# Performance work log

Measured on AMD Instinct MI355X. Metric: run time of the kernel, lower is better.

Reference implementation:

```python
import jax, jax.numpy as jnp
import numpy as np

H = 128          # hidden_channels == num_features for both node types
L = 3            # num_layers
E_TYPES = 3      # (a->a), (a->b), (b->a)
N = 200000       # nodes per type
E = 600000       # edges per edge type
G = 64           # graphs in batch
C = 10           # num_classes
BN_EPS = 1e-5


def setup_inputs() -> dict:
    key = jax.random.key(0)
    ks = jax.random.split(key, 16)
    x_a = jax.random.normal(ks[0], (N, H), dtype=jnp.float32)
    x_b = jax.random.normal(ks[1], (N, H), dtype=jnp.float32)
    ei_aa = jax.random.randint(ks[2], (2, E), 0, N, dtype=jnp.int32)
    ei_ab = jax.random.randint(ks[3], (2, E), 0, N, dtype=jnp.int32)
    ei_ba = jax.random.randint(ks[4], (2, E), 0, N, dtype=jnp.int32)
    batch_a = jnp.sort(jax.random.randint(ks[5], (N,), 0, G, dtype=jnp.int32))
    batch_b = jnp.sort(jax.random.randint(ks[6], (N,), 0, G, dtype=jnp.int32))
    s = 1.0 / np.sqrt(H)
    # GraphConv params per (layer, edge_type): lin_rel (weight+bias), lin_root (no bias)
    Wrel = jax.random.uniform(ks[7], (L, E_TYPES, H, H), jnp.float32, -s, s)
    brel = jax.random.uniform(ks[8], (L, E_TYPES, H), jnp.float32, -s, s)
    Wroot = jax.random.uniform(ks[9], (L, E_TYPES, H, H), jnp.float32, -s, s)
    # BatchNorm affine params per node type (0='a', 1='b')
    bn_gamma = jnp.ones((2, H), jnp.float32)
    bn_beta = jnp.zeros((2, H), jnp.float32)
    lin_W = jax.random.uniform(ks[10], (C, H), jnp.float32, -s, s)
    lin_b = jax.random.uniform(ks[11], (C,), jnp.float32, -s, s)
    return {"x_a": x_a, "x_b": x_b, "Wrel": Wrel, "brel": brel, "Wroot": Wroot,
            "bn_gamma": bn_gamma, "bn_beta": bn_beta, "lin_W": lin_W, "lin_b": lin_b,
            "ei_aa": ei_aa, "ei_ab": ei_ab, "ei_ba": ei_ba,
            "batch_a": batch_a, "batch_b": batch_b}


def _graph_conv(x_src, x_dst, ei, W_rel, b_rel, W_root):
    # PyG GraphConv (aggr='add'): out = lin_rel(sum_{j in N(i)} x_j) + lin_root(x_i)
    agg = jax.ops.segment_sum(x_src[ei[0]], ei[1], num_segments=x_dst.shape[0])
    return agg @ W_rel.T + b_rel + x_dst @ W_root.T


def _bn(x, gamma, beta):
    # BatchNorm in training mode: batch statistics (biased variance)
    mu = x.mean(axis=0)
    var = x.var(axis=0)
    return gamma * (x - mu) * jax.lax.rsqrt(var + BN_EPS) + beta


def reference(x_a, x_b, Wrel, brel, Wroot, bn_gamma, bn_beta, lin_W, lin_b,
              ei_aa, ei_ab, ei_ba, batch_a, batch_b):
    for l in range(L):
        # HeteroConv sums contributions per destination node type
        out_a = (_graph_conv(x_a, x_a, ei_aa, Wrel[l, 0], brel[l, 0], Wroot[l, 0]) +
                 _graph_conv(x_b, x_a, ei_ba, Wrel[l, 2], brel[l, 2], Wroot[l, 2]))
        out_b = _graph_conv(x_a, x_b, ei_ab, Wrel[l, 1], brel[l, 1], Wroot[l, 1])
        x_a = _bn(jax.nn.relu(out_a), bn_gamma[0], bn_beta[0])
        x_b = _bn(jax.nn.relu(out_b), bn_gamma[1], bn_beta[1])
    # global mean pool over concatenated node types
    feats = jnp.concatenate([x_a, x_b], axis=0)
    batch = jnp.concatenate([batch_a, batch_b], axis=0)
    sums = jax.ops.segment_sum(feats, batch, num_segments=G)
    counts = jax.ops.segment_sum(jnp.ones((feats.shape[0],), feats.dtype), batch, num_segments=G)
    pooled = sums / jnp.maximum(counts, 1.0)[:, None]
    return pooled @ lin_W.T + lin_b
```

## Files before the change

### kernel.cpp

```cpp
#include <hip/hip_runtime.h>
#include <hip/hip_bf16.h>

#define HF 128

typedef unsigned int uint32;
typedef unsigned short ushort16;
typedef float f32x4 __attribute__((ext_vector_type(4)));
typedef __bf16 bf16x8 __attribute__((ext_vector_type(8)));

__device__ __forceinline__ float bflo(uint32 u) { return __uint_as_float(u << 16); }
__device__ __forceinline__ float bfhi(uint32 u) { return __uint_as_float(u & 0xffff0000u); }
__device__ __forceinline__ ushort16 f2bf(float f) {
  uint32 u = __float_as_uint(f);
  return (ushort16)((u + 0x7fffu + ((u >> 16) & 1u)) >> 16);
}
__device__ __forceinline__ uint32 pack2(float lo, float hi) {
  return (uint32)f2bf(lo) | ((uint32)f2bf(hi) << 16);
}

__global__ void diag_k(float* __restrict__ out, int n, float val) {
  int i = blockIdx.x * 256 + threadIdx.x;
  if (i < n) out[i] = val;
}

__global__ void init_k(float* __restrict__ ss, float* __restrict__ pool, int Gn) {
  int idx = blockIdx.x * 256 + threadIdx.x;
  if (idx < 512) ss[idx] = (idx < 128 || (idx >= 256 && idx < 384)) ? 1.f : 0.f;
  int p = idx - 512;
  if (p >= 0 && p < Gn * HF) pool[p] = 0.f;
}

__global__ void zrow_k(uint32* __restrict__ a0, uint32* __restrict__ a1,
                       uint32* __restrict__ b, size_t offA, size_t offB) {
  int t = threadIdx.x;
  if (t < 64) a0[offA + t] = 0;
  else if (t < 128) a1[offA + (t - 64)] = 0;
  else if (t < 192) b[offB + (t - 128)] = 0;
}

__global__ void conv_k(const float* __restrict__ in, uint32* __restrict__ out, int n4) {
  int i = blockIdx.x * 256 + threadIdx.x;
  if (i >= n4) return;
  float4 v = ((const float4*)in)[i];
  uint2 p;
  p.x = pack2(v.x, v.y);
  p.y = pack2(v.z, v.w);
  ((uint2*)out)[i] = p;
}

__global__ void initcs_k(int* __restrict__ cs, size_t c0, size_t c1, size_t c2,
                         int vA, int vB) {
  size_t i = ((size_t)blockIdx.x * 256 + threadIdx.x) * 4;
  size_t tot = c0 + c1 + c2;
  if (i >= tot) return;
  int v = (i < c0 + c1) ? vA : vB;
  int4 w = make_int4(v, v, v, v);
  *(int4*)&cs[i] = w;
}

__global__ void count3_k(const int* __restrict__ eA, int EA, int* __restrict__ rA,
                         const int* __restrict__ eB, int EB, int* __restrict__ rB,
                         const int* __restrict__ eC, int EC, int* __restrict__ rC,
                         int B0, int B1) {
  int b = blockIdx.x;
  const int* ei; int E; int* rp;
  if (b < B0)            { ei = eA; E = EA; rp = rA; }
  else if (b < B0 + B1)  { ei = eB; E = EB; rp = rB; b -= B0; }
  else                   { ei = eC; E = EC; rp = rC; b -= B0 + B1; }
  int e = b * 256 + threadIdx.x;
  if (e < E) atomicAdd(&rp[ei[E + e]], 1);
}

__device__ __forceinline__ int pad4(int c) { return (c + 3) & ~3; }

__device__ __forceinline__ void scan1_body(const int* __restrict__ rp, int N,
                                           int* __restrict__ bsum, int b, int t) {
  int i = b * 1024 + t * 4;
  int s = 0;
  if (i + 3 < N) {
    int4 v = *(const int4*)&rp[i];
    s = pad4(v.x) + pad4(v.y) + pad4(v.z) + pad4(v.w);
  } else {
    for (int j = 0; j < 4; ++j) if (i + j < N) s += pad4(rp[i + j]);
  }
  __shared__ int sd[256];
  sd[t] = s;
  __syncthreads();
  for (int o = 128; o > 0; o >>= 1) {
    if (t < o) sd[t] += sd[t + o];
    __syncthreads();
  }
  if (t == 0) bsum[b] = sd[0];
}

__global__ __launch_bounds__(256) void scan1x3_k(
    const int* __restrict__ rA, int NA, int* __restrict__ bA,
    const int* __restrict__ rB, int NB, int* __restrict__ bB,
    const int* __restrict__ rC, int NC, int* __restrict__ bC, int nbA, int nbB) {
  int b = blockIdx.x;
  if (b < nbA)            scan1_body(rA, NA, bA, b, threadIdx.x);
  else if (b < nbA + nbB) scan1_body(rB, NB, bB, b - nbA, threadIdx.x);
  else                    scan1_body(rC, NC, bC, b - nbA - nbB, threadIdx.x);
}

__global__ __launch_bounds__(1024) void scan2x3_k(int* __restrict__ bA, int nbA,
                                                  int* __restrict__ bB, int nbB,
                                                  int* __restrict__ bC, int nbC) {
  int* bsum = (blockIdx.x == 0) ? bA : (blockIdx.x == 1) ? bB : bC;
  int nb    = (blockIdx.x == 0) ? nbA : (blockIdx.x == 1) ? nbB : nbC;
  __shared__ int sd[1024];
  int t = threadIdx.x;
  int v = (t < nb) ? bsum[t] : 0;
  sd[t] = v;
  __syncthreads();
  for (int o = 1; o < 1024; o <<= 1) {
    int x = (t >= o) ? sd[t - o] : 0;
    __syncthreads();
    sd[t] += x;
    __syncthreads();
  }
  if (t < nb) bsum[t] = sd[t] - v;
}

__device__ __forceinline__ void scan3_body(int* __restrict__ rp, int* __restrict__ cur,
                                           int* __restrict__ deg,
                                           const int* __restrict__ bsum, int N,
                                           int b, int t) {
  int i = b * 1024 + t * 4;
  int c[4];
  #pragma unroll
  for (int j = 0; j < 4; ++j) c[j] = (i + j < N) ? rp[i + j] : 0;
  int tsum = pad4(c[0]) + pad4(c[1]) + pad4(c[2]) + pad4(c[3]);
  __shared__ int sd[256];
  sd[t] = tsum;
  __syncthreads();
  for (int o = 1; o < 256; o <<= 1) {
    int x = (t >= o) ? sd[t - o] : 0;
    __syncthreads();
    sd[t] += x;
    __syncthreads();
  }
  int off = bsum[b] + sd[t] - tsum;
  int p = off;
  #pragma unroll
  for (int j = 0; j < 4; ++j) {
    if (i + j < N) { rp[i + j] = p; cur[i + j] = p; deg[i + j] = c[j]; }
    p += pad4(c[j]);
  }
  if (i < N && N <= i + 4) rp[N] = off + tsum;
}

__global__ __launch_bounds__(256) void scan3x3_k(
    int* __restrict__ rA, int* __restrict__ cA, int* __restrict__ dA,
    const int* __restrict__ bA, int NA,
    int* __restrict__ rB, int* __restrict__ cB, int* __restrict__ dB,
    const int* __restrict__ bB, int NB,
    int* __restrict__ rC, int* __restrict__ cC, int* __restrict__ dC,
    const int* __restrict__ bC, int NC,
    int nbA, int nbB) {
  int b = blockIdx.x;
  if (b < nbA)            scan3_body(rA, cA, dA, bA, NA, b, threadIdx.x);
  else if (b < nbA + nbB) scan3_body(rB, cB, dB, bB, NB, b - nbA, threadIdx.x);
  else                    scan3_body(rC, cC, dC, bC, NC, b - nbA - nbB, threadIdx.x);
}

#define FILL_P 4
__global__ __launch_bounds__(256) void fill3p_k(
    const int* __restrict__ eA, int EA, int* __restrict__ cuA, int* __restrict__ csA,
    const int* __restrict__ eB, int EB, int* __restrict__ cuB, int* __restrict__ csB,
    const int* __restrict__ eC, int EC, int* __restrict__ cuC, int* __restrict__ csC,
    int NA, int NBn, int B0, int B1, int Btot) {
  int pass = blockIdx.x / Btot;
  int b = blockIdx.x % Btot;
  const int* ei; int E; int* cur; int* cs; int N;
  if (b < B0)           { ei = eA; E = EA; cur = cuA; cs = csA; N = NA; }
  else if (b < B0 + B1) { ei = eB; E = EB; cur = cuB; cs = csB; N = NBn; b -= B0; }
  else                  { ei = eC; E = EC; cur = cuC; cs = csC; N = NA; b -= B0 + B1; }
  int e = b * 256 + threadIdx.x;
  if (e >= E) return;
  int dst = ei[E + e];
  int lo = (int)(((long long)pass * N) / FILL_P);
  int hi = (int)(((long long)(pass + 1) * N) / FILL_P);
  if (dst < lo || dst >= hi) return;
  int pos = atomicAdd(&cur[dst], 1);
  cs[pos] = ei[e];
}

__global__ __launch_bounds__(128) void prep2_k(
    const float* __restrict__ Wrel_l, const float* __restrict__ Wroot_l,
    const float* __restrict__ brel_l, const float* __restrict__ ss,
    ushort16* __restrict__ BWa, ushort16* __restrict__ BWb,
    float* __restrict__ uvec, float* __restrict__ stats) {
  __shared__ float red[128];
  int n = blockIdx.x, k = threadIdx.x;
  if (n < 64) {
    float4 z = make_float4(0.f, 0.f, 0.f, 0.f);
    *(float4*)&stats[n * 512 + k * 4] = z;
  }
  float scA = ss[k], shA = ss[128 + k], scB = ss[256 + k], shB = ss[384 + k];
  float w0  = Wrel_l[n * HF + k];
  float w1  = Wrel_l[16384 + n * HF + k];
  float w2  = Wrel_l[32768 + n * HF + k];
  float wr1 = Wroot_l[16384 + n * HF + k];
  float wrc = Wroot_l[n * HF + k] + Wroot_l[32768 + n * HF + k];

  int ksl = k >> 5;
  int lane = (n & 15) + (((k >> 3) & 3) << 4);
  int j = k & 7;
  int nt = n >> 4;
  auto put = [&](ushort16* B, int ksb, float v) {
    B[((size_t)((ksb + ksl) * 8 + nt) * 64 + lane) * 8 + j] = f2bf(v);
  };
  put(BWa, 0, scA * w0);
  put(BWa, 4, scB * w2);
  put(BWa, 8, scA * wrc);
  put(BWb, 0, scA * w1);
  put(BWb, 4, scB * wr1);

  auto reduce = [&](float v) -> float {
    red[k] = v;
    __syncthreads();
    for (int s = 64; s > 0; s >>= 1) {
      if (k < s) red[k] += red[k + s];
      __syncthreads();
    }
    float r = red[0];
    __syncthreads();
    return r;
  };
  float r0 = reduce(shA * w0);
  float r1 = reduce(shB * w2);
  float r2 = reduce(shA * w1);
  float r3 = reduce(shA * wrc);
  float r4 = reduce(shB * wr1);
  if (k == 0) {
    uvec[n]       = r0;
    uvec[128 + n] = r1;
    uvec[256 + n] = r2;
    uvec[384 + n] = brel_l[n] + brel_l[256 + n] + r3;
    uvec[512 + n] = brel_l[128 + n] + r4;
  }
}

template <bool HAS2>
__global__ __launch_bounds__(256) void gg_k(
    const uint32* __restrict__ Xg1, const int* __restrict__ rp1, const int* __restrict__ cs1,
    const int* __restrict__ deg1,
    const uint32* __restrict__ Xg2, const int* __restrict__ rp2, const int* __restrict__ cs2,
    const int* __restrict__ deg2,
    const uint32* Xr,
    const bf16x8* __restrict__ BW,
    const float* __restrict__ u1, const float* __restrict__ u2,
    const float* __restrict__ bias,
    uint32* out,
    float* __restrict__ statS, float* __restrict__ statQ,
    int nRows) {
  constexpr int KS_G = HAS2 ? 8 : 4;
  __shared__ uint32 lds[4][1088];
  int tid = threadIdx.x, wid = tid >> 6, l = tid & 63;
  int R0 = blockIdx.x * 64 + wid * 16;
  uint32* L = &lds[wid][0];
  int row = l & 15, khi = l >> 4;
  int myRow = R0 + row;
  bool okRow = myRow < nRows;
  int rowIdx = okRow ? myRow : nRows;

  float lo[16], hi[16];
  auto addv = [&](int base, uint4 v) {
    hi[base + 0] += __uint_as_float(v.x); lo[base + 0] += __uint_as_float(v.x << 16);
    hi[base + 1] += __uint_as_float(v.y); lo[base + 1] += __uint_as_float(v.y << 16);
    hi[base + 2] += __uint_as_float(v.z); lo[base + 2] += __uint_as_float(v.z << 16);
    hi[base + 3] += __uint_as_float(v.w); lo[base + 3] += __uint_as_float(v.w << 16);
  };
  auto gather_reg = [&](const uint32* __restrict__ Xg, const int* __restrict__ rp,
                        const int* __restrict__ cs) {
    #pragma unroll
    for (int i = 0; i < 16; ++i) { lo[i] = 0.f; hi[i] = 0.f; }
    if (okRow) {
      int e0 = rp[myRow], e1 = rp[myRow + 1];
      for (int e = e0; e < e1; e += 4) {
        int i0 = cs[e], i1 = cs[e + 1], i2 = cs[e + 2], i3 = cs[e + 3];
        const uint32* p0 = &Xg[(size_t)i0 * 64 + khi * 4];
        const uint32* p1 = &Xg[(size_t)i1 * 64 + khi * 4];
        const uint32* p2 = &Xg[(size_t)i2 * 64 + khi * 4];
        const uint32* p3 = &Xg[(size_t)i3 * 64 + khi * 4];
        uint4 a0 = *(const uint4*)&p0[0];
        uint4 a1 = *(const uint4*)&p0[16];
        uint4 a2 = *(const uint4*)&p0[32];
        uint4 a3 = *(const uint4*)&p0[48];
        uint4 b0 = *(const uint4*)&p1[0];
        uint4 b1 = *(const uint4*)&p1[16];
        uint4 b2 = *(const uint4*)&p1[32];
        uint4 b3 = *(const uint4*)&p1[48];
        uint4 c0 = *(const uint4*)&p2[0];
        uint4 c1 = *(const uint4*)&p2[16];
        uint4 c2 = *(const uint4*)&p2[32];
        uint4 c3 = *(const uint4*)&p2[48];
        uint4 d0 = *(const uint4*)&p3[0];
        uint4 d1 = *(const uint4*)&p3[16];
        uint4 d2 = *(const uint4*)&p3[32];
        uint4 d3 = *(const uint4*)&p3[48];
        addv(0, a0); addv(4, a1); addv(8, a2); addv(12, a3);
        addv(0, b0); addv(4, b1); addv(8, b2); addv(12, b3);
        addv(0, c0); addv(4, c1); addv(8, c2); addv(12, c3);
        addv(0, d0); addv(4, d1); addv(8, d2); addv(12, d3);
      }
    }
  };
  auto to_frag = [&](int ks) -> bf16x8 {
    bf16x8 a;
    #pragma unroll
    for (int j = 0; j < 4; ++j) {
      a[2 * j]     = (__bf16)lo[ks * 4 + j];
      a[2 * j + 1] = (__bf16)hi[ks * 4 + j];
    }
    return a;
  };

  f32x4 acc[8] = {};
  const bf16x8* Bl = BW + l;

  gather_reg(Xg1, rp1, cs1);
  {
    bf16x8 af[4];
    #pragma unroll
    for (int ks = 0; ks < 4; ++ks) af[ks] = to_frag(ks);
    #pragma unroll
    for (int ks = 0; ks < 4; ++ks) {
      #pragma unroll
      for (int nt = 0; nt < 8; ++nt) {
        bf16x8 b = Bl[(size_t)(ks * 8 + nt) * 64];
        acc[nt] = __builtin_amdgcn_mfma_f32_16x16x32_bf16(af[ks], b, acc[nt], 0, 0, 0);
      }
    }
  }
  if constexpr (HAS2) {
    gather_reg(Xg2, rp2, cs2);
    bf16x8 af[4];
    #pragma unroll
    for (int ks = 0; ks < 4; ++ks) af[ks] = to_frag(ks);
    #pragma unroll
    for (int ks = 0; ks < 4; ++ks) {
      #pragma unroll
      for (int nt = 0; nt < 8; ++nt) {
        bf16x8 b = Bl[(size_t)((4 + ks) * 8 + nt) * 64];
        acc[nt] = __builtin_amdgcn_mfma_f32_16x16x32_bf16(af[ks], b, acc[nt], 0, 0, 0);
      }
    }
  }
  #pragma unroll
  for (int ks = 0; ks < 4; ++ks) {
    bf16x8 a = *(const bf16x8*)&Xr[(size_t)rowIdx * 64 + (ks * 4 + khi) * 4];
    #pragma unroll
    for (int nt = 0; nt < 8; ++nt) {
      bf16x8 b = Bl[(size_t)((KS_G + ks) * 8 + nt) * 64];
      acc[nt] = __builtin_amdgcn_mfma_f32_16x16x32_bf16(a, b, acc[nt], 0, 0, 0);
    }
  }

  int rl0 = khi * 4;
  float deg1v[4], deg2v[4];
  #pragma unroll
  for (int j = 0; j < 4; ++j) {
    int r = R0 + rl0 + j;
    deg1v[j] = (r < nRows) ? (float)deg1[r] : 0.f;
    if constexpr (HAS2) deg2v[j] = (r < nRows) ? (float)deg2[r] : 0.f;
    else deg2v[j] = 0.f;
  }
  ushort16* P = (ushort16*)L;
  int c0 = l & 15;
  float ps[8], pq[8];
  #pragma unroll
  for (int nt = 0; nt < 8; ++nt) {
    int col = nt * 16 + c0;
    float bc = bias[col];
    float u1c = u1[col];
    float u2c = HAS2 ? u2[col] : 0.f;
    float s = 0.f, q = 0.f;
    #pragma unroll
    for (int j = 0; j < 4; ++j) {
      float v = acc[nt][j] + bc + deg1v[j] * u1c;
      if constexpr (HAS2) v += deg2v[j] * u2c;
      v = fmaxf(v, 0.f);
      if (R0 + rl0 + j < nRows) { s += v; q += v * v; }
      P[(rl0 + j) * 136 + col] = f2bf(v);
    }
    ps[nt] = s; pq[nt] = q;
  }

  #pragma unroll
  for (int rr = 0; rr < 4; ++rr) {
    int rloc = rr * 4 + khi;
    int grow = R0 + rloc;
    if (grow < nRows) {
      uint4 v = *(const uint4*)&P[rloc * 136 + c0 * 8];
      *(uint4*)&out[(size_t)grow * 64 + c0 * 4] = v;
    }
  }

  #pragma unroll
  for (int nt = 0; nt < 8; ++nt) {
    ps[nt] += __shfl_xor(ps[nt], 16); ps[nt] += __shfl_xor(ps[nt], 32);
    pq[nt] += __shfl_xor(pq[nt], 16); pq[nt] += __shfl_xor(pq[nt], 32);
  }
  if (l < 16) {
    float* S = statS + (size_t)(blockIdx.x & 63) * 128;
    float* Q = statQ + (size_t)(blockIdx.x & 63) * 128;
    #pragma unroll
    for (int nt = 0; nt < 8; ++nt) {
      unsafeAtomicAdd(&S[nt * 16 + l], ps[nt]);
      unsafeAtomicAdd(&Q[nt * 16 + l], pq[nt]);
    }
  }
}

__global__ void bn_fin_k(const float* __restrict__ stats, const float* __restrict__ gamma,
                         const float* __restrict__ beta, float* __restrict__ ss,
                         float nA, float nB) {
  int t = threadIdx.x;
  if (t >= 256) return;
  int type = t >> 7, f = t & 127;
  const float* S = stats + (size_t)type * 16384;
  const float* Q = S + 8192;
  float s = 0.f, q = 0.f;
  for (int st = 0; st < 64; ++st) { s += S[st * 128 + f]; q += Q[st * 128 + f]; }
  float nN = type ? nB : nA;
  float mean = s / nN;
  float var = q / nN - mean * mean;
  float rstd = rsqrtf(var + 1e-5f);
  float sc = gamma[type * HF + f] * rstd;
  float sh = beta[type * HF + f] - mean * sc;
  ss[type * 256 + f] = sc;
  ss[type * 256 + 128 + f] = sh;
}

__global__ __launch_bounds__(256) void pool_k(const uint32* __restrict__ x,
                                              const int* __restrict__ batch,
                                              const float* __restrict__ scale,
                                              const float* __restrict__ shift,
                                              float* __restrict__ pool, int nN) {
  int f2 = threadIdx.x & 31;
  int sub = threadIdx.x >> 5;
  int start = blockIdx.x * 1024;
  int end = min(start + 1024, nN);
  float4 sc = *(const float4*)&scale[f2 * 4];
  float4 sh = *(const float4*)&shift[f2 * 4];
  float a0 = 0.f, a1 = 0.f, a2 = 0.f, a3 = 0.f, cnt = 0.f;
  int cur = -1;
  for (int n = start + sub; n < end; n += 8) {
    int g = batch[n];
    if (g != cur) {
      if (cur >= 0) {
        float* bp = &pool[(size_t)cur * HF + f2 * 4];
        unsafeAtomicAdd(bp + 0, sc.x * a0 + cnt * sh.x);
        unsafeAtomicAdd(bp + 1, sc.y * a1 + cnt * sh.y);
        unsafeAtomicAdd(bp + 2, sc.z * a2 + cnt * sh.z);
        unsafeAtomicAdd(bp + 3, sc.w * a3 + cnt * sh.w);
      }
      a0 = a1 = a2 = a3 = 0.f; cnt = 0.f; cur = g;
    }
    uint2 v = *(const uint2*)&x[(size_t)n * 64 + f2 * 2];
    a0 += bflo(v.x); a1 += bfhi(v.x); a2 += bflo(v.y); a3 += bfhi(v.y);
    cnt += 1.f;
  }
  if (cur >= 0) {
    float* bp = &pool[(size_t)cur * HF + f2 * 4];
    unsafeAtomicAdd(bp + 0, sc.x * a0 + cnt * sh.x);
    unsafeAtomicAdd(bp + 1, sc.y * a1 + cnt * sh.y);
    unsafeAtomicAdd(bp + 2, sc.z * a2 + cnt * sh.z);
    unsafeAtomicAdd(bp + 3, sc.w * a3 + cnt * sh.w);
  }
}

__device__ inline int lowerb(const int* a, int n, int v) {
  int lo = 0, hi = n;
  while (lo < hi) { int m = (lo + hi) >> 1; if (a[m] < v) lo = m + 1; else hi = m; }
  return lo;
}

__global__ void counts_k(const int* __restrict__ ba, int nA, const int* __restrict__ bb, int nB,
                         float* __restrict__ counts, int Gn) {
  for (int g = threadIdx.x; g < Gn; g += blockDim.x) {
    int c = (lowerb(ba, nA, g + 1) - lowerb(ba, nA, g)) +
            (lowerb(bb, nB, g + 1) - lowerb(bb, nB, g));
    counts[g] = fmaxf((float)c, 1.f);
  }
}

__global__ void final_k(const float* __restrict__ pool, const float* __restrict__ counts,
                        const float* __restrict__ linW, const float* __restrict__ linb,
                        float* __restrict__ out, int Cn) {
  int g = blockIdx.x;
  int lane = threadIdx.x;
  float inv = 1.f / counts[g];
  float p0 = pool[(size_t)g * HF + lane] * inv;
  float p1 = pool[(size_t)g * HF + 64 + lane] * inv;
  for (int c = 0; c < Cn; ++c) {
    float t = p0 * linW[c * HF + lane] + p1 * linW[c * HF + 64 + lane];
    for (int off = 32; off > 0; off >>= 1) t += __shfl_down(t, off);
    if (lane == 0) out[g * Cn + c] = t + linb[c];
  }
}

extern "C" void kernel_launch(void* const* d_in, const int* in_sizes, int n_in,
                              void* d_out, int out_size, void* d_ws, size_t ws_size,
                              hipStream_t stream) {
  const float* x_a   = (const float*)d_in[0];
  const float* x_b   = (const float*)d_in[1];
  const float* Wrel  = (const float*)d_in[2];
  const float* brel  = (const float*)d_in[3];
  const float* Wroot = (const float*)d_in[4];
  const float* bn_g  = (const float*)d_in[5];
  const float* bn_b  = (const float*)d_in[6];
  const float* lin_W = (const float*)d_in[7];
  const float* lin_b = (const float*)d_in[8];
  const int* ei_aa   = (const int*)d_in[9];
  const int* ei_ab   = (const int*)d_in[10];
  const int* ei_ba   = (const int*)d_in[11];
  const int* batch_a = (const int*)d_in[12];
  const int* batch_b = (const int*)d_in[13];

  int Na  = in_sizes[0] / HF;
  int Nb  = in_sizes[1] / HF;
  int Eaa = in_sizes[9] / 2;
  int Eab = in_sizes[10] / 2;
  int Eba = in_sizes[11] / 2;
  int Cn  = in_sizes[7] / HF;
  int Gn  = out_size / Cn;

  size_t NHa = (size_t)Na * HF, NHb = (size_t)Nb * HF;
  size_t capA = ((size_t)Eaa + 3 * (size_t)Na + 15) & ~(size_t)15;
  size_t capB = ((size_t)Eab + 3 * (size_t)Nb + 15) & ~(size_t)15;
  size_t capC = ((size_t)Eba + 3 * (size_t)Na + 15) & ~(size_t)15;

  char* base = (char*)d_ws;
  auto alignup = [](size_t x) { return (x + 255) & ~(size_t)255; };
  size_t off = 0;
  size_t oXA0 = off; off = alignup(off + (NHa + HF) * 2);
  size_t oXA1 = off; off = alignup(off + (NHa + HF) * 2);
  size_t oXB  = off; off = alignup(off + (NHb + HF) * 2);
  size_t oRP  = off; off = alignup(off + ((size_t)(Na + 1) + (Nb + 1) + (Na + 1)) * 4);
  size_t oCUR = off; off = alignup(off + ((size_t)Na + Nb + Na) * 4);
  size_t oDEG = off; off = alignup(off + ((size_t)Na + Nb + Na) * 4);
  size_t oCS  = off; off = alignup(off + (capA + capB + capC) * 4);
  size_t oBWA = off; off = alignup(off + (size_t)12 * 8 * 64 * 16);
  size_t oBWB = off; off = alignup(off + (size_t)8 * 8 * 64 * 16);
  size_t oUV  = off; off = alignup(off + 5 * 128 * 4);
  size_t oSS  = off; off = alignup(off + 512 * 4);
  size_t oST  = off; off = alignup(off + 32768 * 4);
  size_t oBS  = off; off = alignup(off + 3072 * 4);
  size_t oPOOL= off; off = alignup(off + (size_t)Gn * HF * 4);
  size_t oCNT = off; off = alignup(off + (size_t)Gn * 4);
  size_t need = off;

  if (ws_size < need) {
    diag_k<<<(out_size + 255) / 256, 256, 0, stream>>>(
        (float*)d_out, out_size, (float)((double)ws_size / 1048576.0));
    return;
  }

  uint32* XA0 = (uint32*)(base + oXA0);
  uint32* XA1 = (uint32*)(base + oXA1);
  uint32* XB  = (uint32*)(base + oXB);
  int* rp_aa = (int*)(base + oRP);
  int* rp_ab = rp_aa + (Na + 1);
  int* rp_ba = rp_ab + (Nb + 1);
  int* cur_aa = (int*)(base + oCUR);
  int* cur_ab = cur_aa + Na;
  int* cur_ba = cur_ab + Nb;
  int* deg_aa = (int*)(base + oDEG);
  int* deg_ab = deg_aa + Na;
  int* deg_ba = deg_ab + Nb;
  int* cs_aa = (int*)(base + oCS);
  int* cs_ab = cs_aa + capA;
  int* cs_ba = cs_ab + capB;
  ushort16* BWa = (ushort16*)(base + oBWA);
  ushort16* BWb = (ushort16*)(base + oBWB);
  float* uvec  = (float*)(base + oUV);
  float* ss    = (float*)(base + oSS);
  float* stats = (float*)(base + oST);
  int* bsum    = (int*)(base + oBS);
  float* pool  = (float*)(base + oPOOL);
  float* counts= (float*)(base + oCNT);

  float* ss_a = ss;
  float* ss_b = ss + 256;
  float* uaa = uvec, *uba = uvec + 128, *uab = uvec + 256;
  float* bias_a = uvec + 384, *bias_b = uvec + 512;
  float* SA = stats, *QA = stats + 8192, *SB = stats + 16384, *QB = stats + 24576;

  init_k<<<(512 + Gn * HF + 255) / 256, 256, 0, stream>>>(ss, pool, Gn);
  conv_k<<<((int)(NHa / 4) + 255) / 256, 256, 0, stream>>>(x_a, XA0, (int)(NHa / 4));
  conv_k<<<((int)(NHb / 4) + 255) / 256, 256, 0, stream>>>(x_b, XB, (int)(NHb / 4));
  zrow_k<<<1, 256, 0, stream>>>(XA0, XA1, XB, NHa / 2, NHb / 2);

  hipMemsetAsync(rp_aa, 0, ((size_t)(Na + 1) + (Nb + 1) + (Na + 1)) * 4, stream);
  int B0 = (Eaa + 255) / 256, B1 = (Eab + 255) / 256, B2 = (Eba + 255) / 256;
  count3_k<<<B0 + B1 + B2, 256, 0, stream>>>(ei_aa, Eaa, rp_aa, ei_ab, Eab, rp_ab,
                                             ei_ba, Eba, rp_ba, B0, B1);

  int nb_a = (Na + 1023) / 1024;
  int nb_b = (Nb + 1023) / 1024;
  scan1x3_k<<<nb_a + nb_b + nb_a, 256, 0, stream>>>(
      rp_aa, Na, bsum, rp_ab, Nb, bsum + 1024, rp_ba, Na, bsum + 2048, nb_a, nb_b);
  scan2x3_k<<<3, 1024, 0, stream>>>(bsum, nb_a, bsum + 1024, nb_b, bsum + 2048, nb_a);
  scan3x3_k<<<nb_a + nb_b + nb_a, 256, 0, stream>>>(
      rp_aa, cur_aa, deg_aa, bsum, Na,
      rp_ab, cur_ab, deg_ab, bsum + 1024, Nb,
      rp_ba, cur_ba, deg_ba, bsum + 2048, Na, nb_a, nb_b);

  size_t capTot = capA + capB + capC;
  initcs_k<<<(int)((capTot / 4 + 255) / 256), 256, 0, stream>>>(
      cs_aa, capA, capB, capC, Na, Nb);

  int Btot = B0 + B1 + B2;
  fill3p_k<<<FILL_P * Btot, 256, 0, stream>>>(ei_aa, Eaa, cur_aa, cs_aa,
                                              ei_ab, Eab, cur_ab, cs_ab,
                                              ei_ba, Eba, cur_ba, cs_ba,
                                              Na, Nb, B0, B1, Btot);

  uint32* xa_cur = XA0;
  uint32* xa_nxt = XA1;
  for (int l = 0; l < 3; ++l) {
    const float* Wrel_l  = Wrel  + (size_t)l * 3 * 16384;
    const float* Wroot_l = Wroot + (size_t)l * 3 * 16384;
    const float* brel_l  = brel  + (size_t)l * 3 * HF;

    prep2_k<<<128, 128, 0, stream>>>(Wrel_l, Wroot_l, brel_l, ss, BWa, BWb, uvec, stats);

    gg_k<true><<<(Na + 63) / 64, 256, 0, stream>>>(
        xa_cur, rp_aa, cs_aa, deg_aa, XB, rp_ba, cs_ba, deg_ba, xa_cur,
        (const bf16x8*)BWa, uaa, uba, bias_a, xa_nxt, SA, QA, Na);
    gg_k<false><<<(Nb + 63) / 64, 256, 0, stream>>>(
        xa_cur, rp_ab, cs_ab, deg_ab, nullptr, nullptr, nullptr, nullptr, XB,
        (const bf16x8*)BWb, uab, nullptr, bias_b, XB, SB, QB, Nb);

    bn_fin_k<<<1, 256, 0, stream>>>(stats, bn_g, bn_b, ss, (float)Na, (float)Nb);

    uint32* t = xa_cur; xa_cur = xa_nxt; xa_nxt = t;
  }

  pool_k<<<(Na + 1023) / 1024, 256, 0, stream>>>(xa_cur, batch_a, ss_a, ss_a + 128, pool, Na);
  pool_k<<<(Nb + 1023) / 1024, 256, 0, stream>>>(XB, batch_b, ss_b, ss_b + 128, pool, Nb);
  counts_k<<<1, 256, 0, stream>>>(batch_a, Na, batch_b, Nb, counts, Gn);
  final_k<<<Gn, 64, 0, stream>>>(pool, counts, lin_W, lin_b, (float*)d_out, Cn);
}
```

Before: 1.088 ms.

## Fuse setup and BN-finalize kernels, prefetch edge indices in gather

Merges the input-conversion, dummy-row zeroing, CSR index init and pool zeroing kernels into one setup launch. BatchNorm finalization moves into the weight-prep kernel by double-buffering the stats, and graph counts fold into the final linear kernel, cutting per-layer and tail launches. The gather-GEMM kernel now loads CSR neighbour indices as int4 with one-step-ahead prefetch and hoists root-row and degree loads ahead of the gathers to overlap latency. In exchange, prep2 redundantly reduces stats in every block, and register pressure rises from holding both A fragments at once.

```diff
diff --git a/kernel.cpp b/kernel.cpp
--- a/kernel.cpp
+++ b/kernel.cpp
@@ -23,39 +23,54 @@
   if (i < n) out[i] = val;
 }
 
-__global__ void init_k(float* __restrict__ ss, float* __restrict__ pool, int Gn) {
-  int idx = blockIdx.x * 256 + threadIdx.x;
-  if (idx < 512) ss[idx] = (idx < 128 || (idx >= 256 && idx < 384)) ? 1.f : 0.f;
-  int p = idx - 512;
-  if (p >= 0 && p < Gn * HF) pool[p] = 0.f;
-}
-
-__global__ void zrow_k(uint32* __restrict__ a0, uint32* __restrict__ a1,
-                       uint32* __restrict__ b, size_t offA, size_t offB) {
-  int t = threadIdx.x;
-  if (t < 64) a0[offA + t] = 0;
-  else if (t < 128) a1[offA + (t - 64)] = 0;
-  else if (t < 192) b[offB + (t - 128)] = 0;
-}
-
-__global__ void conv_k(const float* __restrict__ in, uint32* __restrict__ out, int n4) {
-  int i = blockIdx.x * 256 + threadIdx.x;
-  if (i >= n4) return;
-  float4 v = ((const float4*)in)[i];
-  uint2 p;
-  p.x = pack2(v.x, v.y);
-  p.y = pack2(v.z, v.w);
-  ((uint2*)out)[i] = p;
-}
-
-__global__ void initcs_k(int* __restrict__ cs, size_t c0, size_t c1, size_t c2,
-                         int vA, int vB) {
-  size_t i = ((size_t)blockIdx.x * 256 + threadIdx.x) * 4;
-  size_t tot = c0 + c1 + c2;
-  if (i >= tot) return;
-  int v = (i < c0 + c1) ? vA : vB;
-  int4 w = make_int4(v, v, v, v);
-  *(int4*)&cs[i] = w;
+__global__ __launch_bounds__(256) void setup_k(
+    const float* __restrict__ xa, const float* __restrict__ xb,
+    uint32* __restrict__ XA0, uint32* __restrict__ XA1, uint32* __restrict__ XB,
+    int n4a, int n4b,
+    int* __restrict__ cs, size_t capA, size_t capB, size_t capC, int vA, int vB,
+    float* __restrict__ pool, int poolN4,
+    size_t dummyA, size_t dummyB,
+    int CA, int CB, int CI, int PZ) {
+  int b = blockIdx.x, t = threadIdx.x;
+  if (b < CA) {
+    int i = b * 256 + t;
+    if (i < n4a) {
+      float4 v = ((const float4*)xa)[i];
+      uint2 p; p.x = pack2(v.x, v.y); p.y = pack2(v.z, v.w);
+      ((uint2*)XA0)[i] = p;
+    }
+    return;
+  }
+  b -= CA;
+  if (b < CB) {
+    int i = b * 256 + t;
+    if (i < n4b) {
+      float4 v = ((const float4*)xb)[i];
+      uint2 p; p.x = pack2(v.x, v.y); p.y = pack2(v.z, v.w);
+      ((uint2*)XB)[i] = p;
+    }
+    return;
+  }
+  b -= CB;
+  if (b < CI) {
+    size_t i = ((size_t)b * 256 + t) * 4;
+    size_t tot = capA + capB + capC;
+    if (i < tot) {
+      int v = (i < capA + capB) ? vA : vB;
+      int4 w = make_int4(v, v, v, v);
+      *(int4*)&cs[i] = w;
+    }
+    return;
+  }
+  b -= CI;
+  if (b < PZ) {
+    int i = b * 256 + t;
+    if (i < poolN4) ((float4*)pool)[i] = make_float4(0.f, 0.f, 0.f, 0.f);
+    return;
+  }
+  if (t < 64) XA0[dummyA + t] = 0;
+  else if (t < 128) XA1[dummyA + (t - 64)] = 0;
+  else if (t < 192) XB[dummyB + (t - 128)] = 0;
 }
 
 __global__ void count3_k(const int* __restrict__ eA, int EA, int* __restrict__ rA,
@@ -188,16 +203,36 @@
 
 __global__ __launch_bounds__(128) void prep2_k(
     const float* __restrict__ Wrel_l, const float* __restrict__ Wroot_l,
-    const float* __restrict__ brel_l, const float* __restrict__ ss,
+    const float* __restrict__ brel_l,
+    const float* __restrict__ gamma, const float* __restrict__ beta,
+    const float* __restrict__ statsPrev, float* __restrict__ statsNext,
+    float nA, float nB, int first,
     ushort16* __restrict__ BWa, ushort16* __restrict__ BWb,
-    float* __restrict__ uvec, float* __restrict__ stats) {
+    float* __restrict__ uvec) {
   __shared__ float red[128];
   int n = blockIdx.x, k = threadIdx.x;
+  float scA, shA, scB, shB;
+  if (first) {
+    scA = 1.f; shA = 0.f; scB = 1.f; shB = 0.f;
+  } else {
+    float sA = 0.f, qA = 0.f, sB = 0.f, qB = 0.f;
+    for (int st = 0; st < 64; ++st) {
+      sA += statsPrev[st * 128 + k];
+      qA += statsPrev[8192 + st * 128 + k];
+      sB += statsPrev[16384 + st * 128 + k];
+      qB += statsPrev[24576 + st * 128 + k];
+    }
+    float mA = sA / nA, vA = qA / nA - mA * mA;
+    float rA = rsqrtf(vA + 1e-5f);
+    scA = gamma[k] * rA; shA = beta[k] - mA * scA;
+    float mB = sB / nB, vB = qB / nB - mB * mB;
+    float rB = rsqrtf(vB + 1e-5f);
+    scB = gamma[128 + k] * rB; shB = beta[128 + k] - mB * scB;
+  }
   if (n < 64) {
     float4 z = make_float4(0.f, 0.f, 0.f, 0.f);
-    *(float4*)&stats[n * 512 + k * 4] = z;
-  }
-  float scA = ss[k], shA = ss[128 + k], scB = ss[256 + k], shB = ss[384 + k];
+    *(float4*)&statsNext[n * 512 + k * 4] = z;
+  }
   float w0  = Wrel_l[n * HF + k];
   float w1  = Wrel_l[16384 + n * HF + k];
   float w2  = Wrel_l[32768 + n * HF + k];
@@ -265,6 +300,28 @@
   bool okRow = myRow < nRows;
   int rowIdx = okRow ? myRow : nRows;
 
+  int e0a = 0, e1a = 0;
+  if (okRow) { e0a = rp1[myRow]; e1a = rp1[myRow + 1]; }
+  int e0b = 0, e1b = 0;
+  if constexpr (HAS2) { if (okRow) { e0b = rp2[myRow]; e1b = rp2[myRow + 1]; } }
+  bf16x8 rt[4];
+  #pragma unroll
+  for (int ks = 0; ks < 4; ++ks)
+    rt[ks] = *(const bf16x8*)&Xr[(size_t)rowIdx * 64 + (ks * 4 + khi) * 4];
+  int4 q1 = make_int4(0, 0, 0, 0), q2 = make_int4(0, 0, 0, 0);
+  if (e0a < e1a) q1 = *(const int4*)&cs1[e0a];
+  if constexpr (HAS2) { if (e0b < e1b) q2 = *(const int4*)&cs2[e0b]; }
+  int rl0 = khi * 4;
+  float dg1[4] = {0.f, 0.f, 0.f, 0.f}, dg2[4] = {0.f, 0.f, 0.f, 0.f};
+  #pragma unroll
+  for (int j = 0; j < 4; ++j) {
+    int r = R0 + rl0 + j;
+    if (r < nRows) {
+      dg1[j] = (float)deg1[r];
+      if constexpr (HAS2) dg2[j] = (float)deg2[r];
+    }
+  }
+
   float lo[16], hi[16];
   auto addv = [&](int base, uint4 v) {
     hi[base + 0] += __uint_as_float(v.x); lo[base + 0] += __uint_as_float(v.x << 16);
@@ -272,39 +329,44 @@
     hi[base + 2] += __uint_as_float(v.z); lo[base + 2] += __uint_as_float(v.z << 16);
     hi[base + 3] += __uint_as_float(v.w); lo[base + 3] += __uint_as_float(v.w << 16);
   };
-  auto gather_reg = [&](const uint32* __restrict__ Xg, const int* __restrict__ rp,
-                        const int* __restrict__ cs) {
+  auto run_tile = [&](const uint32* __restrict__ Xg, const int* __restrict__ cs,
+                      int e0, int e1, int4 qinit) {
     #pragma unroll
     for (int i = 0; i < 16; ++i) { lo[i] = 0.f; hi[i] = 0.f; }
-    if (okRow) {
-      int e0 = rp[myRow], e1 = rp[myRow + 1];
-      for (int e = e0; e < e1; e += 4) {
-        int i0 = cs[e], i1 = cs[e + 1], i2 = cs[e + 2], i3 = cs[e + 3];
-        const uint32* p0 = &Xg[(size_t)i0 * 64 + khi * 4];
-        const uint32* p1 = &Xg[(size_t)i1 * 64 + khi * 4];
-        const uint32* p2 = &Xg[(size_t)i2 * 64 + khi * 4];
-        const uint32* p3 = &Xg[(size_t)i3 * 64 + khi * 4];
-        uint4 a0 = *(const uint4*)&p0[0];
-        uint4 a1 = *(const uint4*)&p0[16];
-        uint4 a2 = *(const uint4*)&p0[32];
-        uint4 a3 = *(const uint4*)&p0[48];
-        uint4 b0 = *(const uint4*)&p1[0];
-        uint4 b1 = *(const uint4*)&p1[16];
-        uint4 b2 = *(const uint4*)&p1[32];
-        uint4 b3 = *(const uint4*)&p1[48];
-        uint4 c0 = *(const uint4*)&p2[0];
-        uint4 c1 = *(const uint4*)&p2[16];
-        uint4 c2 = *(const uint4*)&p2[32];
-        uint4 c3 = *(const uint4*)&p2[48];
-        uint4 d0 = *(const uint4*)&p3[0];
-        uint4 d1 = *(const uint4*)&p3[16];
-        uint4 d2 = *(const uint4*)&p3[32];
-        uint4 d3 = *(const uint4*)&p3[48];
-        addv(0, a0); addv(4, a1); addv(8, a2); addv(12, a3);
-        addv(0, b0); addv(4, b1); addv(8, b2); addv(12, b3);
-        addv(0, c0); addv(4, c1); addv(8, c2); addv(12, c3);
-        addv(0, d0); addv(4, d1); addv(8, d2); addv(12, d3);
-      }
+    if (e0 >= e1) return;
+    int e = e0;
+    int4 q = qinit;
+    for (;;) {
+      const uint32* p0 = &Xg[(size_t)q.x * 64 + khi * 4];
+      const uint32* p1 = &Xg[(size_t)q.y * 64 + khi * 4];
+      const uint32* p2 = &Xg[(size_t)q.z * 64 + khi * 4];
+      const uint32* p3 = &Xg[(size_t)q.w * 64 + khi * 4];
+      uint4 a0 = *(const uint4*)&p0[0];
+      uint4 a1 = *(const uint4*)&p0[16];
+      uint4 a2 = *(const uint4*)&p0[32];
+      uint4 a3 = *(const uint4*)&p0[48];
+      uint4 b0 = *(const uint4*)&p1[0];
+      uint4 b1 = *(const uint4*)&p1[16];
+      uint4 b2 = *(const uint4*)&p1[32];
+      uint4 b3 = *(const uint4*)&p1[48];
+      uint4 c0 = *(const uint4*)&p2[0];
+      uint4 c1 = *(const uint4*)&p2[16];
+      uint4 c2 = *(const uint4*)&p2[32];
+      uint4 c3 = *(const uint4*)&p2[48];
+      uint4 d0 = *(const uint4*)&p3[0];
+      uint4 d1 = *(const uint4*)&p3[16];
+      uint4 d2 = *(const uint4*)&p3[32];
+      uint4 d3 = *(const uint4*)&p3[48];
+      int en = e + 4;
+      bool more = en < e1;
+      int4 qn = q;
+      if (more) qn = *(const int4*)&cs[en];
+      addv(0, a0); addv(4, a1); addv(8, a2); addv(12, a3);
+      addv(0, b0); addv(4, b1); addv(8, b2); addv(12, b3);
+      addv(0, c0); addv(4, c1); addv(8, c2); addv(12, c3);
+      addv(0, d0); addv(4, d1); addv(8, d2); addv(12, d3);
+      if (!more) break;
+      e = en; q = qn;
     }
   };
   auto to_frag = [&](int ks) -> bf16x8 {
@@ -317,56 +379,47 @@
     return a;
   };
 
+  run_tile(Xg1, cs1, e0a, e1a, q1);
+  bf16x8 af1[4];
+  #pragma unroll
+  for (int ks = 0; ks < 4; ++ks) af1[ks] = to_frag(ks);
+
+  bf16x8 af2[4];
+  if constexpr (HAS2) {
+    run_tile(Xg2, cs2, e0b, e1b, q2);
+    #pragma unroll
+    for (int ks = 0; ks < 4; ++ks) af2[ks] = to_frag(ks);
+  }
+
   f32x4 acc[8] = {};
   const bf16x8* Bl = BW + l;
-
-  gather_reg(Xg1, rp1, cs1);
-  {
-    bf16x8 af[4];
+  #pragma unroll
+  for (int ks = 0; ks < 4; ++ks) {
     #pragma unroll
-    for (int ks = 0; ks < 4; ++ks) af[ks] = to_frag(ks);
-    #pragma unroll
-    for (int ks = 0; ks < 4; ++ks) {
-      #pragma unroll
-      for (int nt = 0; nt < 8; ++nt) {
-        bf16x8 b = Bl[(size_t)(ks * 8 + nt) * 64];
-        acc[nt] = __builtin_amdgcn_mfma_f32_16x16x32_bf16(af[ks], b, acc[nt], 0, 0, 0);
-      }
+    for (int nt = 0; nt < 8; ++nt) {
+      bf16x8 b = Bl[(size_t)(ks * 8 + nt) * 64];
+      acc[nt] = __builtin_amdgcn_mfma_f32_16x16x32_bf16(af1[ks], b, acc[nt], 0, 0, 0);
     }
   }
   if constexpr (HAS2) {
-    gather_reg(Xg2, rp2, cs2);
-    bf16x8 af[4];
-    #pragma unroll
-    for (int ks = 0; ks < 4; ++ks) af[ks] = to_frag(ks);
     #pragma unroll
     for (int ks = 0; ks < 4; ++ks) {
       #pragma unroll
       for (int nt = 0; nt < 8; ++nt) {
         bf16x8 b = Bl[(size_t)((4 + ks) * 8 + nt) * 64];
-        acc[nt] = __builtin_amdgcn_mfma_f32_16x16x32_bf16(af[ks], b, acc[nt], 0, 0, 0);
+        acc[nt] = __builtin_amdgcn_mfma_f32_16x16x32_bf16(af2[ks], b, acc[nt], 0, 0, 0);
       }
     }
   }
   #pragma unroll
   for (int ks = 0; ks < 4; ++ks) {
-    bf16x8 a = *(const bf16x8*)&Xr[(size_t)rowIdx * 64 + (ks * 4 + khi) * 4];
     #pragma unroll
     for (int nt = 0; nt < 8; ++nt) {
       bf16x8 b = Bl[(size_t)((KS_G + ks) * 8 + nt) * 64];
-      acc[nt] = __builtin_amdgcn_mfma_f32_16x16x32_bf16(a, b, acc[nt], 0, 0, 0);
-    }
-  }
-
-  int rl0 = khi * 4;
-  float deg1v[4], deg2v[4];
-  #pragma unroll
-  for (int j = 0; j < 4; ++j) {
-    int r = R0 + rl0 + j;
-    deg1v[j] = (r < nRows) ? (float)deg1[r] : 0.f;
-    if constexpr (HAS2) deg2v[j] = (r < nRows) ? (float)deg2[r] : 0.f;
-    else deg2v[j] = 0.f;
-  }
+      acc[nt] = __builtin_amdgcn_mfma_f32_16x16x32_bf16(rt[ks], b, acc[nt], 0, 0, 0);
+    }
+  }
+
   ushort16* P = (ushort16*)L;
   int c0 = l & 15;
   float ps[8], pq[8];
@@ -379,8 +432,8 @@
     float s = 0.f, q = 0.f;
     #pragma unroll
     for (int j = 0; j < 4; ++j) {
-      float v = acc[nt][j] + bc + deg1v[j] * u1c;
-      if constexpr (HAS2) v += deg2v[j] * u2c;
+      float v = acc[nt][j] + bc + dg1[j] * u1c;
+      if constexpr (HAS2) v += dg2[j] * u2c;
       v = fmaxf(v, 0.f);
       if (R0 + rl0 + j < nRows) { s += v; q += v * v; }
       P[(rl0 + j) * 136 + col] = f2bf(v);
@@ -478,27 +531,22 @@
   return lo;
 }
 
-__global__ void counts_k(const int* __restrict__ ba, int nA, const int* __restrict__ bb, int nB,
-                         float* __restrict__ counts, int Gn) {
-  for (int g = threadIdx.x; g < Gn; g += blockDim.x) {
-    int c = (lowerb(ba, nA, g + 1) - lowerb(ba, nA, g)) +
-            (lowerb(bb, nB, g + 1) - lowerb(bb, nB, g));
-    counts[g] = fmaxf((float)c, 1.f);
-  }
-}
-
-__global__ void final_k(const float* __restrict__ pool, const float* __restrict__ counts,
+__global__ void final_k(const float* __restrict__ pool,
+                        const int* __restrict__ ba, int nA,
+                        const int* __restrict__ bb, int nB,
                         const float* __restrict__ linW, const float* __restrict__ linb,
                         float* __restrict__ out, int Cn) {
   int g = blockIdx.x;
   int lane = threadIdx.x;
-  float inv = 1.f / counts[g];
+  int c = (lowerb(ba, nA, g + 1) - lowerb(ba, nA, g)) +
+          (lowerb(bb, nB, g + 1) - lowerb(bb, nB, g));
+  float inv = 1.f / fmaxf((float)c, 1.f);
   float p0 = pool[(size_t)g * HF + lane] * inv;
   float p1 = pool[(size_t)g * HF + 64 + lane] * inv;
-  for (int c = 0; c < Cn; ++c) {
-    float t = p0 * linW[c * HF + lane] + p1 * linW[c * HF + 64 + lane];
+  for (int cc = 0; cc < Cn; ++cc) {
+    float t = p0 * linW[cc * HF + lane] + p1 * linW[cc * HF + 64 + lane];
     for (int off = 32; off > 0; off >>= 1) t += __shfl_down(t, off);
-    if (lane == 0) out[g * Cn + c] = t + linb[c];
+    if (lane == 0) out[g * Cn + cc] = t + linb[cc];
   }
 }
 
@@ -547,10 +595,9 @@
   size_t oBWB = off; off = alignup(off + (size_t)8 * 8 * 64 * 16);
   size_t oUV  = off; off = alignup(off + 5 * 128 * 4);
   size_t oSS  = off; off = alignup(off + 512 * 4);
-  size_t oST  = off; off = alignup(off + 32768 * 4);
+  size_t oST  = off; off = alignup(off + 65536 * 4);
   size_t oBS  = off; off = alignup(off + 3072 * 4);
   size_t oPOOL= off; off = alignup(off + (size_t)Gn * HF * 4);
-  size_t oCNT = off; off = alignup(off + (size_t)Gn * 4);
   size_t need = off;
 
   if (ws_size < need) {
@@ -581,18 +628,22 @@
   float* stats = (float*)(base + oST);
   int* bsum    = (int*)(base + oBS);
   float* pool  = (float*)(base + oPOOL);
-  float* counts= (float*)(base + oCNT);
 
   float* ss_a = ss;
   float* ss_b = ss + 256;
   float* uaa = uvec, *uba = uvec + 128, *uab = uvec + 256;
   float* bias_a = uvec + 384, *bias_b = uvec + 512;
-  float* SA = stats, *QA = stats + 8192, *SB = stats + 16384, *QB = stats + 24576;
-
-  init_k<<<(512 + Gn * HF + 255) / 256, 256, 0, stream>>>(ss, pool, Gn);
-  conv_k<<<((int)(NHa / 4) + 255) / 256, 256, 0, stream>>>(x_a, XA0, (int)(NHa / 4));
-  conv_k<<<((int)(NHb / 4) + 255) / 256, 256, 0, stream>>>(x_b, XB, (int)(NHb / 4));
-  zrow_k<<<1, 256, 0, stream>>>(XA0, XA1, XB, NHa / 2, NHb / 2);
+
+  int n4a = (int)(NHa / 4), n4b = (int)(NHb / 4);
+  int CA = (n4a + 255) / 256, CB = (n4b + 255) / 256;
+  size_t capTot = capA + capB + capC;
+  int CI = (int)((capTot / 4 + 255) / 256);
+  int poolN4 = Gn * HF / 4;
+  int PZ = (poolN4 + 255) / 256;
+  setup_k<<<CA + CB + CI + PZ + 1, 256, 0, stream>>>(
+      x_a, x_b, XA0, XA1, XB, n4a, n4b,
+      cs_aa, capA, capB, capC, Na, Nb,
+      pool, poolN4, NHa / 2, NHb / 2, CA, CB, CI, PZ);
 
   hipMemsetAsync(rp_aa, 0, ((size_t)(Na + 1) + (Nb + 1) + (Na + 1)) * 4, stream);
   int B0 = (Eaa + 255) / 256, B1 = (Eab + 255) / 256, B2 = (Eba + 255) / 256;
@@ -609,10 +660,6 @@
       rp_ab, cur_ab, deg_ab, bsum + 1024, Nb,
       rp_ba, cur_ba, deg_ba, bsum + 2048, Na, nb_a, nb_b);
 
-  size_t capTot = capA + capB + capC;
-  initcs_k<<<(int)((capTot / 4 + 255) / 256), 256, 0, stream>>>(
-      cs_aa, capA, capB, capC, Na, Nb);
-
   int Btot = B0 + B1 + B2;
   fill3p_k<<<FILL_P * Btot, 256, 0, stream>>>(ei_aa, Eaa, cur_aa, cs_aa,
                                               ei_ab, Eab, cur_ab, cs_ab,
@@ -625,23 +672,29 @@
     const float* Wrel_l  = Wrel  + (size_t)l * 3 * 16384;
     const float* Wroot_l = Wroot + (size_t)l * 3 * 16384;
     const float* brel_l  = brel  + (size_t)l * 3 * HF;
-
-    prep2_k<<<128, 128, 0, stream>>>(Wrel_l, Wroot_l, brel_l, ss, BWa, BWb, uvec, stats);
+    float* statsCur  = stats + (size_t)(l & 1) * 32768;
+    float* statsPrev = stats + (size_t)((l + 1) & 1) * 32768;
+
+    prep2_k<<<128, 128, 0, stream>>>(Wrel_l, Wroot_l, brel_l, bn_g, bn_b,
+                                     statsPrev, statsCur, (float)Na, (float)Nb,
+                                     (l == 0) ? 1 : 0, BWa, BWb, uvec);
 
     gg_k<true><<<(Na + 63) / 64, 256, 0, stream>>>(
         xa_cur, rp_aa, cs_aa, deg_aa, XB, rp_ba, cs_ba, deg_ba, xa_cur,
-        (const bf16x8*)BWa, uaa, uba, bias_a, xa_nxt, SA, QA, Na);
+        (const bf16x8*)BWa, uaa, uba, bias_a, xa_nxt,
+        statsCur, statsCur + 8192, Na);
     gg_k<false><<<(Nb + 63) / 64, 256, 0, stream>>>(
         xa_cur, rp_ab, cs_ab, deg_ab, nullptr, nullptr, nullptr, nullptr, XB,
-        (const bf16x8*)BWb, uab, nullptr, bias_b, XB, SB, QB, Nb);
-
-    bn_fin_k<<<1, 256, 0, stream>>>(stats, bn_g, bn_b, ss, (float)Na, (float)Nb);
+        (const bf16x8*)BWb, uab, nullptr, bias_b, XB,
+        statsCur + 16384, statsCur + 24576, Nb);
 
     uint32* t = xa_cur; xa_cur = xa_nxt; xa_nxt = t;
   }
+
+  bn_fin_k<<<1, 256, 0, stream>>>(stats, bn_g, bn_b, ss, (float)Na, (float)Nb);
 
   pool_k<<<(Na + 1023) / 1024, 256, 0, stream>>>(xa_cur, batch_a, ss_a, ss_a + 128, pool, Na);
   pool_k<<<(Nb + 1023) / 1024, 256, 0, stream>>>(XB, batch_b, ss_b, ss_b + 128, pool, Nb);
-  counts_k<<<1, 256, 0, stream>>>(batch_a, Na, batch_b, Nb, counts, Gn);
-  final_k<<<Gn, 64, 0, stream>>>(pool, counts, lin_W, lin_b, (float*)d_out, Cn);
-}
+  final_k<<<Gn, 64, 0, stream>>>(pool, batch_a, Na, batch_b, Nb,
+                                 lin_W, lin_b, (float*)d_out, Cn);
+}
```

Result: faster. 969.4 us (-10.9%).
